# Performance work log

Measured on AMD Instinct MI355X. Metric: run time of the kernel, lower is better.

The kernel has to match this reference:

```python
import jax, jax.numpy as jnp
import numpy as np

ALPHA = 1.0
NEG = -1e20  # boundary value used by the torch module


def _compute_mu(W, alpha):
    """DTW location parameter mu: [B, Na+1, Nb+1].
    mu[i,j] = alpha*W[i-1,j-1] + logsumexp(mu[i-1,j], mu[i,j-1], mu[i-1,j-1]).
    Row-wise scan (outer over i) with an inner scan over j for the
    left-dependency; fully vectorized over batch.
    """
    B, Na, Nb = W.shape
    aW = alpha * W  # [B, Na, Nb]
    # row 0: mu[:,0,0]=0, mu[:,0,1:]=-1e20
    row0 = jnp.concatenate([jnp.zeros((B, 1), W.dtype),
                            jnp.full((B, Nb), NEG, W.dtype)], axis=1)

    def row_step(prev_row, w_row):  # prev_row [B, Nb+1], w_row [B, Nb]
        up = prev_row[:, 1:]    # mu[i-1, j]   for j=1..Nb -> [B, Nb]
        diag = prev_row[:, :-1]  # mu[i-1, j-1]            -> [B, Nb]

        def col_step(left, inp):
            u, d, w = inp  # each [B]
            val = w + jax.nn.logsumexp(jnp.stack([u, left, d], axis=0), axis=0)
            return val, val

        left0 = jnp.full((B,), NEG, W.dtype)  # mu[i, 0] = -1e20
        xs = (up.T, diag.T, w_row.T)          # scan over Nb
        _, vals = jax.lax.scan(col_step, left0, xs)  # [Nb, B]
        new_row = jnp.concatenate([jnp.full((B, 1), NEG, W.dtype), vals.T], axis=1)
        return new_row, new_row

    _, rows = jax.lax.scan(row_step, row0, jnp.swapaxes(aW, 0, 1))  # [Na, B, Nb+1]
    mu = jnp.concatenate([row0[:, None, :], jnp.swapaxes(rows, 0, 1)], axis=1)
    return mu  # [B, Na+1, Nb+1]


def _compute_pi(W, mu, mask, alpha):
    """Reduced transition tensor pi: [B, Na, Nb, 3] (softmax over moves)."""
    up = mu[:, :-1, 1:]    # mu[i-1, j]
    left = mu[:, 1:, :-1]  # mu[i, j-1]
    diag = mu[:, :-1, :-1]  # mu[i-1, j-1]
    raw = jnp.stack([up, left, diag], axis=-1) + alpha * W[..., None]
    return jax.nn.softmax(raw, axis=-1) * mask


def setup_inputs() -> dict:
    key = jax.random.key(0)
    k1, _ = jax.random.split(key)
    B, Na, Nb = 64, 384, 384
    W = jax.random.normal(k1, (B, Na, Nb), dtype=jnp.float32)
    mask = jnp.ones((B, Na, Nb, 1), dtype=jnp.float32)
    return {"W": W, "mask": mask}


def reference(W, mask):
    mu = _compute_mu(W, ALPHA)
    pi = _compute_pi(W, mu, mask, ALPHA)
    return (mu, pi)
```

## Files before the change

kernel.cpp:

```cpp
#include <hip/hip_runtime.h>

#define NA 384
#define NB 384
#define NBATCH 64
#define NEGV -1e20f
#define C 16
#define NCW 6
#define TOT_CH 28
#define WPITCH 68
#define SP 17
#define LOG2E 1.44269504088896340736f
#define LN2   0.69314718055994530942f
#define MUP (NB + 1)

typedef float f4 __attribute__((ext_vector_type(4)));

struct alignas(16) SharedT {
    float stage[2][NCW][64 * SP];
    float wtile[3][NCW][16 * WPITCH];
    float bound[NCW - 1][NB + 1];
    int   progress[NCW - 1];
    int   computed[NCW];
    int   drained[NCW][2];
    int   wready[NCW];
};

__device__ __forceinline__ void loadW16(const float* __restrict__ Wb, int rbase,
                                        int k, int l, float (&r)[16])
{
    const int rl = l >> 3, cc = l & 7;
#pragma unroll
    for (int h = 0; h < 2; ++h) {
        const int colb = 8 * (2 * k + h) + cc;
#pragma unroll
        for (int i = 0; i < 8; ++i) {
            const int row = 8 * i + rl;
            int col = colb - row;
            col = col < 0 ? 0 : (col > NB - 1 ? NB - 1 : col);
            r[8 * h + i] = Wb[(size_t)(rbase + row) * NB + col];
        }
    }
}

__device__ __forceinline__ void writeWt16(float* __restrict__ wt,
                                          const float (&r)[16], int l) {
#pragma unroll
    for (int i = 0; i < 16; ++i) wt[i * WPITCH + l] = r[i] * LOG2E;
}

__device__ __forceinline__ void readWc16(const float* __restrict__ wt, int l,
                                         float (&wc)[16]) {
    const int wb = (l >> 3) * WPITCH + (l & 7) * 8;
    const f4 a = *(const f4*)(wt + wb);
    const f4 b = *(const f4*)(wt + wb + 4);
    const f4 c2 = *(const f4*)(wt + 8 * WPITCH + wb);
    const f4 d = *(const f4*)(wt + 8 * WPITCH + wb + 4);
    wc[0] = a.x;  wc[1] = a.y;  wc[2] = a.z;  wc[3] = a.w;
    wc[4] = b.x;  wc[5] = b.y;  wc[6] = b.z;  wc[7] = b.w;
    wc[8] = c2.x; wc[9] = c2.y; wc[10] = c2.z; wc[11] = c2.w;
    wc[12] = d.x; wc[13] = d.y; wc[14] = d.z; wc[15] = d.w;
}

template<bool FULL>
__device__ __forceinline__ void chunk_body(int k, int w, int l,
        float (&wc)[16], float& val, float& diag, float& m2, SharedT& sh)
{
    const int s0 = 1 + k * C;

    if (k >= 2) {
        volatile int* dr = &sh.drained[w][k & 1];
        while (*dr < k - 2) __builtin_amdgcn_s_sleep(1);
        __builtin_amdgcn_sched_barrier(0);
        asm volatile("" ::: "memory");
    }
    if (w > 0 && s0 <= NB) {
        const int need = (s0 + C - 1 < NB) ? s0 + C - 1 : NB;
        volatile int* pr = &sh.progress[w - 1];
        while (*pr < need) { }
        __builtin_amdgcn_sched_barrier(0);
        asm volatile("" ::: "memory");
    }
    float bnd[C];
    if (w > 0) {
#pragma unroll
        for (int c = 0; c < C; ++c) {
            const int s = s0 + c;
            bnd[c] = sh.bound[w - 1][s <= NB ? s : NB];
        }
    }

    float nvreg[C] = {};
    __builtin_amdgcn_s_setprio(1);
#pragma unroll
    for (int c = 0; c < C; ++c) {
        const int s = s0 + c;
        float upv = __int_as_float(__builtin_amdgcn_update_dpp(
            0, __float_as_int(val), 0x138 , 0xF, 0xF, false));
        if (l == 0) upv = (w > 0 && s <= NB) ? bnd[c] : NEGV;
        const int j = s - l;
        if (FULL || (j >= 1 && j <= NB)) {
            const float m  = fmaxf(upv, m2);
            const float mw = m + wc[c];
            const float eu = exp2f(upv  - m);
            const float el = exp2f(val  - m);
            const float ed = exp2f(diag - m);
            const float nv = mw + __log2f((eu + el) + ed);
            nvreg[c] = nv;
            m2   = fmaxf(nv, upv);
            diag = upv;
            val  = nv;
        }
    }

    if (w < NCW - 1) {
        if (l == 63) {
#pragma unroll
            for (int c = 0; c < C; ++c) {
                const int j63 = s0 + c - 63;
                if (j63 >= 1 && j63 <= NB) sh.bound[w][j63] = nvreg[c];
            }
        }
        asm volatile("s_waitcnt lgkmcnt(0)" ::: "memory");
        if (l == 63) {
            const int done = s0 + C - 1 - 63;
            if (done >= 1) *(volatile int*)&sh.progress[w] = done;
        }
    }
    __builtin_amdgcn_s_setprio(0);

    float* st = &sh.stage[k & 1][w][0] + l * SP;
#pragma unroll
    for (int c = 0; c < C; ++c) st[c] = nvreg[c];
    asm volatile("s_waitcnt lgkmcnt(0)" ::: "memory");
    if (l == 63) *(volatile int*)&sh.computed[w] = k + 1;

    if (k + 1 < TOT_CH) {
        volatile int* wr = &sh.wready[w];
        while (*wr < k + 2) { }
        __builtin_amdgcn_sched_barrier(0);
        asm volatile("" ::: "memory");
        readWc16(&sh.wtile[(k + 1) % 3][w][0], l, wc);
    }
}

template<bool FULL>
__device__ __forceinline__ void io_iter(int k, int cw, int l,
        const float* __restrict__ Wb, int rbase, float* __restrict__ mub,
        float (&wreg)[16], SharedT& sh)
{
    volatile int* cp = &sh.computed[cw];
    while (*cp < k + 1) __builtin_amdgcn_s_sleep(8);
    __builtin_amdgcn_sched_barrier(0);
    asm volatile("" ::: "memory");

    const float* st = &sh.stage[k & 1][cw][0];
    const int lr = l >> 4, cc = l & 15;
    float v[16];
#pragma unroll
    for (int q = 0; q < 16; ++q) v[q] = st[(lr + 4 * q) * SP + cc];
    asm volatile("s_waitcnt lgkmcnt(0)" ::: "memory");
    if (l == 0) *(volatile int*)&sh.drained[cw][k & 1] = k;

    if (k + 3 < TOT_CH) {
        writeWt16(&sh.wtile[(k + 3) % 3][cw][0], wreg, l);
        asm volatile("s_waitcnt lgkmcnt(0)" ::: "memory");
        if (l == 0) *(volatile int*)&sh.wready[cw] = k + 4;
        if (k + 5 < TOT_CH) loadW16(Wb, rbase, k + 5, l, wreg);
    }

    const int colbase = k * C;
#pragma unroll
    for (int q = 0; q < 16; ++q) {
        const int row = lr + 4 * q;
        const int col = colbase + cc - row;
        if (FULL || (unsigned)col < (unsigned)NB)
            mub[(size_t)(rbase + row + 1) * MUP + col + 1] = v[q] * LN2;
    }
}

__global__ __launch_bounds__(768, 1) void dtw_mu(const float* __restrict__ W,
                                                 float* __restrict__ mu)
{
    __shared__ SharedT sh;
    const int b = blockIdx.x, tid = threadIdx.x;
    const int w = tid >> 6, l = tid & 63;
    const float* Wb = W + (size_t)b * NA * NB;
    float* mub = mu + (size_t)b * MUP * MUP;

    if (tid < 384) {
        mub[tid + 1] = NEGV;
        mub[(size_t)(tid + 1) * MUP] = NEGV;
    }
    if (tid == 0) mub[0] = 0.0f;
    if (tid < NCW - 1) sh.progress[tid] = 0;
    if (tid < NCW) { sh.computed[tid] = 0; sh.wready[tid] = 0; }
    if (tid < 2 * NCW) sh.drained[tid >> 1][tid & 1] = -1;
    __syncthreads();

    if (w < NCW) {
        const int rbase = w << 6;
        float val  = NEGV;
        float diag = (rbase + l == 0) ? 0.0f : NEGV;
        float m2   = fmaxf(val, diag);
        float wc[16];
        {
            volatile int* wr = &sh.wready[w];
            while (*wr < 1) { }
            __builtin_amdgcn_sched_barrier(0);
            asm volatile("" ::: "memory");
            readWc16(&sh.wtile[0][w][0], l, wc);
        }
        for (int k = 0; k < 4; ++k)       chunk_body<false>(k, w, l, wc, val, diag, m2, sh);
        for (int k = 4; k < 24; ++k)      chunk_body<true >(k, w, l, wc, val, diag, m2, sh);
        for (int k = 24; k < TOT_CH; ++k) chunk_body<false>(k, w, l, wc, val, diag, m2, sh);
    } else {
        const int cw = w - NCW, rbase = cw << 6;
        float r0[16], rA[16], rB[16];
        loadW16(Wb, rbase, 0, l, r0);
        writeWt16(&sh.wtile[0][cw][0], r0, l);
        loadW16(Wb, rbase, 1, l, r0);
        writeWt16(&sh.wtile[1][cw][0], r0, l);
        loadW16(Wb, rbase, 2, l, r0);
        writeWt16(&sh.wtile[2][cw][0], r0, l);
        loadW16(Wb, rbase, 3, l, rA);
        loadW16(Wb, rbase, 4, l, rB);
        asm volatile("s_waitcnt lgkmcnt(0)" ::: "memory");
        if (l == 0) *(volatile int*)&sh.wready[cw] = 3;

        for (int k = 0; k < 4; k += 2) {
            io_iter<false>(k,     cw, l, Wb, rbase, mub, rA, sh);
            io_iter<false>(k + 1, cw, l, Wb, rbase, mub, rB, sh);
        }
        for (int k = 4; k < 24; k += 2) {
            io_iter<true >(k,     cw, l, Wb, rbase, mub, rA, sh);
            io_iter<true >(k + 1, cw, l, Wb, rbase, mub, rB, sh);
        }
        for (int k = 24; k < TOT_CH; k += 2) {
            io_iter<false>(k,     cw, l, Wb, rbase, mub, rA, sh);
            io_iter<false>(k + 1, cw, l, Wb, rbase, mub, rB, sh);
        }
    }
}

__global__ __launch_bounds__(256) void dtw_pi(const float* __restrict__ W,
        const float* __restrict__ mask, const float* __restrict__ mu,
        float* __restrict__ pi)
{
    const long long idx = ((long long)blockIdx.x * 256 + threadIdx.x) * 4;
    const int rr = (int)(idx / NB);
    const int jj = (int)(idx - (long long)rr * NB);
    const int b  = rr / NA;
    const int ii = rr - b * NA;
    const float* m0 = mu + (size_t)b * MUP * MUP + (size_t)ii * MUP + jj;
    const float* m1 = m0 + MUP;
    const float d0 = m0[0], d1 = m0[1], d2 = m0[2], d3 = m0[3], d4 = m0[4];
    const float L0 = m1[0], L1 = m1[1], L2 = m1[2], L3 = m1[3], L4 = m1[4];
    const f4 wv = *(const f4*)(W + idx);
    const f4 mk = *(const f4*)(mask + idx);

    const float t0 = wv.x - L1, t1 = wv.y - L2, t2 = wv.z - L3, t3 = wv.w - L4;
    f4 o0, o1, o2;
    o0.x = exp2f((d1 + t0) * LOG2E) * mk.x;
    o0.y = exp2f((L0 + t0) * LOG2E) * mk.x;
    o0.z = exp2f((d0 + t0) * LOG2E) * mk.x;
    o0.w = exp2f((d2 + t1) * LOG2E) * mk.y;
    o1.x = exp2f((L1 + t1) * LOG2E) * mk.y;
    o1.y = exp2f((d1 + t1) * LOG2E) * mk.y;
    o1.z = exp2f((d3 + t2) * LOG2E) * mk.z;
    o1.w = exp2f((L2 + t2) * LOG2E) * mk.z;
    o2.x = exp2f((d2 + t2) * LOG2E) * mk.z;
    o2.y = exp2f((d4 + t3) * LOG2E) * mk.w;
    o2.z = exp2f((L3 + t3) * LOG2E) * mk.w;
    o2.w = exp2f((d3 + t3) * LOG2E) * mk.w;

    f4* po = (f4*)(pi + idx * 3);
    po[0] = o0; po[1] = o1; po[2] = o2;
}

extern "C" void kernel_launch(void* const* d_in, const int* in_sizes, int n_in,
                              void* d_out, int out_size, void* d_ws, size_t ws_size,
                              hipStream_t stream) {
    const float* W    = (const float*)d_in[0];
    const float* mask = (const float*)d_in[1];
    float* mu = (float*)d_out;
    float* pi = mu + (size_t)NBATCH * MUP * MUP;

    hipLaunchKernelGGL(dtw_mu, dim3(NBATCH), dim3(768), 0, stream, W, mu);

    const int cells  = NBATCH * NA * NB;
    const int blocks = cells / (256 * 4);
    hipLaunchKernelGGL(dtw_pi, dim3(blocks), dim3(256), 0, stream,
                       W, mask, mu, pi);
}
```

Measured before the change: 143.2 us.

## Assign two DTW rows per lane, halving compute wavefronts to three

Each lane now computes two consecutive rows of the DTW recurrence, so three compute wavefronts each cover 128 rows where six covered 64. The block shrinks from 768 to 384 threads. W tiles are widened to 128 rows with a swizzled shared layout, and the staging and store paths are adapted to match. This cuts inter-wave handoffs and cross-lane DPP hops, but each wave runs a longer serial dependency chain per chunk, so the wavefront pipeline fills more slowly and has less latency hiding.

```diff
diff --git a/kernel.cpp b/kernel.cpp
--- a/kernel.cpp
+++ b/kernel.cpp
@@ -5,10 +5,10 @@
 #define NBATCH 64
 #define NEGV -1e20f
 #define C 16
-#define NCW 6
+#define NCW 3
 #define TOT_CH 28
-#define WPITCH 68
-#define SP 17
+#define WP 20
+#define SP 33
 #define LOG2E 1.44269504088896340736f
 #define LN2   0.69314718055994530942f
 #define MUP (NB + 1)
@@ -17,7 +17,7 @@
 
 struct alignas(16) SharedT {
     float stage[2][NCW][64 * SP];
-    float wtile[3][NCW][16 * WPITCH];
+    float wtile[3][NCW][128 * WP];
     float bound[NCW - 1][NB + 1];
     int   progress[NCW - 1];
     int   computed[NCW];
@@ -25,45 +25,61 @@
     int   wready[NCW];
 };
 
-__device__ __forceinline__ void loadW16(const float* __restrict__ Wb, int rbase,
-                                        int k, int l, float (&r)[16])
+__device__ __forceinline__ void loadW32(const float* __restrict__ Wb, int bb,
+                                        int kk, int l, float (&r)[32])
 {
     const int rl = l >> 3, cc = l & 7;
 #pragma unroll
-    for (int h = 0; h < 2; ++h) {
-        const int colb = 8 * (2 * k + h) + cc;
-#pragma unroll
-        for (int i = 0; i < 8; ++i) {
-            const int row = 8 * i + rl;
-            int col = colb - row;
+    for (int i = 0; i < 16; ++i) {
+        const int row = 8 * i + rl;
+        const int cb = 16 * kk + cc - (row >> 1);
+#pragma unroll
+        for (int h = 0; h < 2; ++h) {
+            int col = cb + 8 * h;
             col = col < 0 ? 0 : (col > NB - 1 ? NB - 1 : col);
-            r[8 * h + i] = Wb[(size_t)(rbase + row) * NB + col];
-        }
-    }
-}
-
-__device__ __forceinline__ void writeWt16(float* __restrict__ wt,
-                                          const float (&r)[16], int l) {
-#pragma unroll
-    for (int i = 0; i < 16; ++i) wt[i * WPITCH + l] = r[i] * LOG2E;
-}
-
-__device__ __forceinline__ void readWc16(const float* __restrict__ wt, int l,
-                                         float (&wc)[16]) {
-    const int wb = (l >> 3) * WPITCH + (l & 7) * 8;
-    const f4 a = *(const f4*)(wt + wb);
-    const f4 b = *(const f4*)(wt + wb + 4);
-    const f4 c2 = *(const f4*)(wt + 8 * WPITCH + wb);
-    const f4 d = *(const f4*)(wt + 8 * WPITCH + wb + 4);
-    wc[0] = a.x;  wc[1] = a.y;  wc[2] = a.z;  wc[3] = a.w;
-    wc[4] = b.x;  wc[5] = b.y;  wc[6] = b.z;  wc[7] = b.w;
-    wc[8] = c2.x; wc[9] = c2.y; wc[10] = c2.z; wc[11] = c2.w;
-    wc[12] = d.x; wc[13] = d.y; wc[14] = d.z; wc[15] = d.w;
+            r[2 * i + h] = Wb[(size_t)(bb + row) * NB + col];
+        }
+    }
+}
+
+__device__ __forceinline__ void writeWt32(float* __restrict__ wt,
+                                          const float (&r)[32], int l)
+{
+    const int rl = l >> 3, cc = l & 7;
+#pragma unroll
+    for (int i = 0; i < 16; ++i) {
+        const int row = 8 * i + rl;
+        const int sw4 = (row >> 4) & 3;
+#pragma unroll
+        for (int h = 0; h < 2; ++h) {
+            const int c = cc + 8 * h;
+            wt[row * WP + 4 * ((c >> 2) ^ sw4) + (c & 3)] = r[2 * i + h] * LOG2E;
+        }
+    }
+}
+
+__device__ __forceinline__ void readW2(const float* __restrict__ wt, int L,
+                                       float (&wcA)[16], float (&wcB)[16])
+{
+    const int sw = (L >> 3) & 3;
+    const float* pA = wt + (2 * L) * WP;
+    const float* pB = wt + (2 * L + 1) * WP;
+#pragma unroll
+    for (int cb = 0; cb < 4; ++cb) {
+        const f4 a = *(const f4*)(pA + 4 * (cb ^ sw));
+        const f4 b = *(const f4*)(pB + 4 * (cb ^ sw));
+        wcA[4 * cb + 0] = a.x; wcA[4 * cb + 1] = a.y;
+        wcA[4 * cb + 2] = a.z; wcA[4 * cb + 3] = a.w;
+        wcB[4 * cb + 0] = b.x; wcB[4 * cb + 1] = b.y;
+        wcB[4 * cb + 2] = b.z; wcB[4 * cb + 3] = b.w;
+    }
 }
 
 template<bool FULL>
 __device__ __forceinline__ void chunk_body(int k, int w, int l,
-        float (&wc)[16], float& val, float& diag, float& m2, SharedT& sh)
+        float (&wcA)[16], float (&wcB)[16],
+        float& valA, float& valB, float& diagA, float& m2A, float& m2B,
+        SharedT& sh)
 {
     const int s0 = 1 + k * C;
 
@@ -89,26 +105,34 @@
         }
     }
 
-    float nvreg[C] = {};
+    float nvAr[C] = {}, nvBr[C] = {};
     __builtin_amdgcn_s_setprio(1);
 #pragma unroll
     for (int c = 0; c < C; ++c) {
         const int s = s0 + c;
-        float upv = __int_as_float(__builtin_amdgcn_update_dpp(
-            0, __float_as_int(val), 0x138 , 0xF, 0xF, false));
-        if (l == 0) upv = (w > 0 && s <= NB) ? bnd[c] : NEGV;
+        float upA = __int_as_float(__builtin_amdgcn_update_dpp(
+            0, __float_as_int(valB), 0x138 , 0xF, 0xF, false));
+        if (l == 0) upA = (w > 0 && s <= NB) ? bnd[c] : NEGV;
         const int j = s - l;
         if (FULL || (j >= 1 && j <= NB)) {
-            const float m  = fmaxf(upv, m2);
-            const float mw = m + wc[c];
-            const float eu = exp2f(upv  - m);
-            const float el = exp2f(val  - m);
-            const float ed = exp2f(diag - m);
-            const float nv = mw + __log2f((eu + el) + ed);
-            nvreg[c] = nv;
-            m2   = fmaxf(nv, upv);
-            diag = upv;
-            val  = nv;
+            const float mA  = fmaxf(upA, m2A);
+            const float mwA = mA + wcA[c];
+            const float a1 = exp2f(upA   - mA);
+            const float a2 = exp2f(valA  - mA);
+            const float a3 = exp2f(diagA - mA);
+            const float nvA = mwA + __log2f((a1 + a2) + a3);
+            const float mB  = fmaxf(nvA, m2B);
+            const float mwB = mB + wcB[c];
+            const float b1 = exp2f(nvA  - mB);
+            const float b2 = exp2f(valB - mB);
+            const float b3 = exp2f(valA - mB);
+            const float nvB = mwB + __log2f((b1 + b2) + b3);
+            nvAr[c] = nvA; nvBr[c] = nvB;
+            m2A = fmaxf(nvA, upA);
+            m2B = fmaxf(nvB, nvA);
+            diagA = upA;
+            valA  = nvA;
+            valB  = nvB;
         }
     }
 
@@ -117,7 +141,7 @@
 #pragma unroll
             for (int c = 0; c < C; ++c) {
                 const int j63 = s0 + c - 63;
-                if (j63 >= 1 && j63 <= NB) sh.bound[w][j63] = nvreg[c];
+                if (j63 >= 1 && j63 <= NB) sh.bound[w][j63] = nvBr[c];
             }
         }
         asm volatile("s_waitcnt lgkmcnt(0)" ::: "memory");
@@ -130,7 +154,10 @@
 
     float* st = &sh.stage[k & 1][w][0] + l * SP;
 #pragma unroll
-    for (int c = 0; c < C; ++c) st[c] = nvreg[c];
+    for (int c = 0; c < C; ++c) {
+        st[2 * c]     = nvAr[c];
+        st[2 * c + 1] = nvBr[c];
+    }
     asm volatile("s_waitcnt lgkmcnt(0)" ::: "memory");
     if (l == 63) *(volatile int*)&sh.computed[w] = k + 1;
 
@@ -139,14 +166,14 @@
         while (*wr < k + 2) { }
         __builtin_amdgcn_sched_barrier(0);
         asm volatile("" ::: "memory");
-        readWc16(&sh.wtile[(k + 1) % 3][w][0], l, wc);
+        readW2(&sh.wtile[(k + 1) % 3][w][0], l, wcA, wcB);
     }
 }
 
 template<bool FULL>
 __device__ __forceinline__ void io_iter(int k, int cw, int l,
-        const float* __restrict__ Wb, int rbase, float* __restrict__ mub,
-        float (&wreg)[16], SharedT& sh)
+        const float* __restrict__ Wb, int bb, float* __restrict__ mub,
+        float (&wreg)[32], SharedT& sh)
 {
     volatile int* cp = &sh.computed[cw];
     while (*cp < k + 1) __builtin_amdgcn_s_sleep(8);
@@ -155,30 +182,32 @@
 
     const float* st = &sh.stage[k & 1][cw][0];
     const int lr = l >> 4, cc = l & 15;
-    float v[16];
-#pragma unroll
-    for (int q = 0; q < 16; ++q) v[q] = st[(lr + 4 * q) * SP + cc];
+    float v[32];
+#pragma unroll
+    for (int q = 0; q < 32; ++q) {
+        const int r = lr + 4 * q;
+        v[q] = st[(r >> 1) * SP + 2 * cc + (r & 1)];
+    }
     asm volatile("s_waitcnt lgkmcnt(0)" ::: "memory");
     if (l == 0) *(volatile int*)&sh.drained[cw][k & 1] = k;
 
     if (k + 3 < TOT_CH) {
-        writeWt16(&sh.wtile[(k + 3) % 3][cw][0], wreg, l);
+        writeWt32(&sh.wtile[(k + 3) % 3][cw][0], wreg, l);
         asm volatile("s_waitcnt lgkmcnt(0)" ::: "memory");
         if (l == 0) *(volatile int*)&sh.wready[cw] = k + 4;
-        if (k + 5 < TOT_CH) loadW16(Wb, rbase, k + 5, l, wreg);
-    }
-
-    const int colbase = k * C;
-#pragma unroll
-    for (int q = 0; q < 16; ++q) {
-        const int row = lr + 4 * q;
-        const int col = colbase + cc - row;
-        if (FULL || (unsigned)col < (unsigned)NB)
-            mub[(size_t)(rbase + row + 1) * MUP + col + 1] = v[q] * LN2;
-    }
-}
-
-__global__ __launch_bounds__(768, 1) void dtw_mu(const float* __restrict__ W,
+        if (k + 5 < TOT_CH) loadW32(Wb, bb, k + 5, l, wreg);
+    }
+
+#pragma unroll
+    for (int q = 0; q < 32; ++q) {
+        const int r = lr + 4 * q;
+        const int j = 16 * k + 1 + cc - (r >> 1);
+        if (FULL || ((unsigned)(j - 1) < (unsigned)NB))
+            mub[(size_t)(bb + r + 1) * MUP + j] = v[q] * LN2;
+    }
+}
+
+__global__ __launch_bounds__(384, 1) void dtw_mu(const float* __restrict__ W,
                                                  float* __restrict__ mu)
 {
     __shared__ SharedT sh;
@@ -187,10 +216,8 @@
     const float* Wb = W + (size_t)b * NA * NB;
     float* mub = mu + (size_t)b * MUP * MUP;
 
-    if (tid < 384) {
-        mub[tid + 1] = NEGV;
-        mub[(size_t)(tid + 1) * MUP] = NEGV;
-    }
+    mub[tid + 1] = NEGV;
+    mub[(size_t)(tid + 1) * MUP] = NEGV;
     if (tid == 0) mub[0] = 0.0f;
     if (tid < NCW - 1) sh.progress[tid] = 0;
     if (tid < NCW) { sh.computed[tid] = 0; sh.wready[tid] = 0; }
@@ -198,46 +225,50 @@
     __syncthreads();
 
     if (w < NCW) {
-        const int rbase = w << 6;
-        float val  = NEGV;
-        float diag = (rbase + l == 0) ? 0.0f : NEGV;
-        float m2   = fmaxf(val, diag);
-        float wc[16];
+        float valA = NEGV, valB = NEGV;
+        float diagA = (w == 0 && l == 0) ? 0.0f : NEGV;
+        float m2A = fmaxf(valA, diagA);
+        float m2B = NEGV;
+        float wcA[16], wcB[16];
         {
             volatile int* wr = &sh.wready[w];
             while (*wr < 1) { }
             __builtin_amdgcn_sched_barrier(0);
             asm volatile("" ::: "memory");
-            readWc16(&sh.wtile[0][w][0], l, wc);
-        }
-        for (int k = 0; k < 4; ++k)       chunk_body<false>(k, w, l, wc, val, diag, m2, sh);
-        for (int k = 4; k < 24; ++k)      chunk_body<true >(k, w, l, wc, val, diag, m2, sh);
-        for (int k = 24; k < TOT_CH; ++k) chunk_body<false>(k, w, l, wc, val, diag, m2, sh);
+            readW2(&sh.wtile[0][w][0], l, wcA, wcB);
+        }
+        for (int k = 0; k < 4; ++k)
+            chunk_body<false>(k, w, l, wcA, wcB, valA, valB, diagA, m2A, m2B, sh);
+        for (int k = 4; k < 24; ++k)
+            chunk_body<true >(k, w, l, wcA, wcB, valA, valB, diagA, m2A, m2B, sh);
+        for (int k = 24; k < TOT_CH; ++k)
+            chunk_body<false>(k, w, l, wcA, wcB, valA, valB, diagA, m2A, m2B, sh);
     } else {
-        const int cw = w - NCW, rbase = cw << 6;
-        float r0[16], rA[16], rB[16];
-        loadW16(Wb, rbase, 0, l, r0);
-        writeWt16(&sh.wtile[0][cw][0], r0, l);
-        loadW16(Wb, rbase, 1, l, r0);
-        writeWt16(&sh.wtile[1][cw][0], r0, l);
-        loadW16(Wb, rbase, 2, l, r0);
-        writeWt16(&sh.wtile[2][cw][0], r0, l);
-        loadW16(Wb, rbase, 3, l, rA);
-        loadW16(Wb, rbase, 4, l, rB);
+        const int cw = w - NCW;
+        const int bb = cw << 7;
+        float r0[32], rA[32], rB[32];
+        loadW32(Wb, bb, 0, l, r0);
+        writeWt32(&sh.wtile[0][cw][0], r0, l);
+        loadW32(Wb, bb, 1, l, r0);
+        writeWt32(&sh.wtile[1][cw][0], r0, l);
+        loadW32(Wb, bb, 2, l, r0);
+        writeWt32(&sh.wtile[2][cw][0], r0, l);
+        loadW32(Wb, bb, 3, l, rA);
+        loadW32(Wb, bb, 4, l, rB);
         asm volatile("s_waitcnt lgkmcnt(0)" ::: "memory");
         if (l == 0) *(volatile int*)&sh.wready[cw] = 3;
 
         for (int k = 0; k < 4; k += 2) {
-            io_iter<false>(k,     cw, l, Wb, rbase, mub, rA, sh);
-            io_iter<false>(k + 1, cw, l, Wb, rbase, mub, rB, sh);
+            io_iter<false>(k,     cw, l, Wb, bb, mub, rA, sh);
+            io_iter<false>(k + 1, cw, l, Wb, bb, mub, rB, sh);
         }
         for (int k = 4; k < 24; k += 2) {
-            io_iter<true >(k,     cw, l, Wb, rbase, mub, rA, sh);
-            io_iter<true >(k + 1, cw, l, Wb, rbase, mub, rB, sh);
+            io_iter<true >(k,     cw, l, Wb, bb, mub, rA, sh);
+            io_iter<true >(k + 1, cw, l, Wb, bb, mub, rB, sh);
         }
         for (int k = 24; k < TOT_CH; k += 2) {
-            io_iter<false>(k,     cw, l, Wb, rbase, mub, rA, sh);
-            io_iter<false>(k + 1, cw, l, Wb, rbase, mub, rB, sh);
+            io_iter<false>(k,     cw, l, Wb, bb, mub, rA, sh);
+            io_iter<false>(k + 1, cw, l, Wb, bb, mub, rB, sh);
         }
     }
 }
@@ -285,7 +316,7 @@
     float* mu = (float*)d_out;
     float* pi = mu + (size_t)NBATCH * MUP * MUP;
 
-    hipLaunchKernelGGL(dtw_mu, dim3(NBATCH), dim3(768), 0, stream, W, mu);
+    hipLaunchKernelGGL(dtw_mu, dim3(NBATCH), dim3(384), 0, stream, W, mu);
 
     const int cells  = NBATCH * NA * NB;
     const int blocks = cells / (256 * 4);
```

Result: slower. 298.3 us (+108.3%).
